# Optimization experiments

Hardware: AMD Instinct MI355X
Metric: run time of the kernel (lower is better)

The kernel has to match this reference:

```python
import jax, jax.numpy as jnp
import numpy as np

EPS = 1e-5

def setup_inputs() -> dict:
    key = jax.random.key(0)
    ks = jax.random.split(key, 12)
    B, S = 48, 1024
    x = jax.random.normal(ks[0], (3, B, S, 3), dtype=jnp.float32)
    # stacked per-band projection weights: index 0=a, 1=b, 2=c
    WQ = jax.random.normal(ks[1], (3, 3, 3), dtype=jnp.float32) * 0.3
    bQ = jax.random.normal(ks[2], (3, 3), dtype=jnp.float32) * 0.1
    WK = jax.random.normal(ks[3], (3, 3, 3), dtype=jnp.float32) * 0.3
    bK = jax.random.normal(ks[4], (3, 3), dtype=jnp.float32) * 0.1
    WV = jax.random.normal(ks[5], (3, 3, 3), dtype=jnp.float32) * 0.3
    bV = jax.random.normal(ks[6], (3, 3), dtype=jnp.float32) * 0.1
    bn_gamma = jnp.ones((9,), dtype=jnp.float32)
    bn_beta = jnp.zeros((9,), dtype=jnp.float32)
    fc_w = jax.random.normal(ks[7], (3, 9), dtype=jnp.float32) * 0.3
    fc_b = jax.random.normal(ks[8], (3,), dtype=jnp.float32) * 0.1
    return dict(x=x, WQ=WQ, bQ=bQ, WK=WK, bK=bK, WV=WV, bV=bV,
                bn_gamma=bn_gamma, bn_beta=bn_beta, fc_w=fc_w, fc_b=fc_b)

def _attn(Q, K, V):
    # Q,K,V: (B, S, 3)
    scores = jnp.einsum('bsd,btd->bst', Q, K) / jnp.sqrt(jnp.float32(3.0))
    w = jax.nn.softmax(scores, axis=-1)
    return jnp.einsum('bst,btd->bsd', w, V)

def reference(x, WQ, bQ, WK, bK, WV, bV, bn_gamma, bn_beta, fc_w, fc_b):
    # x: (3, B, S, 3) -> per-band xs[n]: (B, S, 3)
    xs = x  # band axis already leading
    # per-band projections: Q[n] = xs[n] @ WQ[n].T + bQ[n]
    Q = jnp.einsum('nbsd,ned->nbse', xs, WQ) + bQ[:, None, None, :]
    K = jnp.einsum('nbsd,ned->nbse', xs, WK) + bK[:, None, None, :]
    V = jnp.einsum('nbsd,ned->nbse', xs, WV) + bV[:, None, None, :]
    a1 = _attn(Q[2], K[0], V[1])  # Q_c, K_a, V_b
    a2 = _attn(Q[0], K[1], V[2])  # Q_a, K_b, V_c
    a3 = _attn(Q[1], K[2], V[0])  # Q_b, K_c, V_a
    out = jnp.concatenate([a1, a2, a3], axis=-1)  # (B, S, 9)
    flat = out.reshape(-1, 9)
    # BatchNorm1d (training-mode batch statistics, biased variance)
    mean = jnp.mean(flat, axis=0)
    var = jnp.var(flat, axis=0)
    normed = (flat - mean) / jnp.sqrt(var + EPS) * bn_gamma + bn_beta
    y = normed @ fc_w.T + fc_b  # (B*S, 3)
    return y.reshape(-1, 3, 3)
```

## Files before the change

### kernel.cpp

```cpp
#include <hip/hip_runtime.h>
#include <math.h>

#define BB 48
#define SS 1024
#define NCB (3 * BB)
#define NROW (BB * SS)
#define NBLK2 (NROW / 256)

typedef float f32x2 __attribute__((ext_vector_type(2)));


template <int KSv>
__global__ __launch_bounds__(256) void mbfca_attn(
    const float* __restrict__ x,
    const float* __restrict__ WQ, const float* __restrict__ bQ,
    const float* __restrict__ WK, const float* __restrict__ bK,
    const float* __restrict__ WV, const float* __restrict__ bV,
    float* __restrict__ part)
{
    constexpr int SSK = SS / KSv;
    const int bid   = blockIdx.x;
    const int slice = bid % KSv;
    const int cb    = bid / KSv;
    const int c     = cb / BB;
    const int b     = cb % BB;
    const int kband = c;
    const int vband = (c + 1) % 3;
    const int qband = (c + 2) % 3;

    __shared__ __align__(16) float Ksm[3][SSK];
    __shared__ __align__(16) float Vsm[3][SSK];

    const int tid = threadIdx.x;

    float wk[9], wv[9], wq[9], bk[3], bv[3], bq[3];
    #pragma unroll
    for (int i = 0; i < 9; ++i) {
        wk[i] = WK[kband * 9 + i];
        wv[i] = WV[vband * 9 + i];
        wq[i] = WQ[qband * 9 + i];
    }
    #pragma unroll
    for (int i = 0; i < 3; ++i) {
        bk[i] = bK[kband * 3 + i];
        bv[i] = bV[vband * 3 + i];
        bq[i] = bQ[qband * 3 + i];
    }

    const float* xk = x + (size_t)(kband * BB + b) * SS * 3;
    const float* xv = x + (size_t)(vband * BB + b) * SS * 3;
    const float* xq = x + (size_t)(qband * BB + b) * SS * 3;

    for (int t = tid; t < SSK; t += 256) {
        const int tk = slice * SSK + t;
        float a0 = xk[tk * 3 + 0], a1 = xk[tk * 3 + 1], a2 = xk[tk * 3 + 2];
        Ksm[0][t] = wk[0] * a0 + wk[1] * a1 + wk[2] * a2 + bk[0];
        Ksm[1][t] = wk[3] * a0 + wk[4] * a1 + wk[5] * a2 + bk[1];
        Ksm[2][t] = wk[6] * a0 + wk[7] * a1 + wk[8] * a2 + bk[2];
        float c0 = xv[tk * 3 + 0], c1 = xv[tk * 3 + 1], c2 = xv[tk * 3 + 2];
        Vsm[0][t] = wv[0] * c0 + wv[1] * c1 + wv[2] * c2 + bv[0];
        Vsm[1][t] = wv[3] * c0 + wv[4] * c1 + wv[5] * c2 + bv[1];
        Vsm[2][t] = wv[6] * c0 + wv[7] * c1 + wv[8] * c2 + bv[2];
    }
    __syncthreads();

    const float qscale = 0.57735026918962576f * 1.4426950408889634f;
    f32x2 qp0[4], qp1[4], qp2[4];
    {
        const float4* xq4 = reinterpret_cast<const float4*>(xq + 12 * tid);
        float4 A = xq4[0], B4 = xq4[1], C4 = xq4[2];
        float a[12] = {A.x, A.y, A.z, A.w, B4.x, B4.y, B4.z, B4.w,
                       C4.x, C4.y, C4.z, C4.w};
        #pragma unroll
        for (int j = 0; j < 4; ++j) {
            float a0 = a[j * 3 + 0], a1 = a[j * 3 + 1], a2 = a[j * 3 + 2];
            float t0 = (wq[0] * a0 + wq[1] * a1 + wq[2] * a2 + bq[0]) * qscale;
            float t1 = (wq[3] * a0 + wq[4] * a1 + wq[5] * a2 + bq[1]) * qscale;
            float t2 = (wq[6] * a0 + wq[7] * a1 + wq[8] * a2 + bq[2]) * qscale;
            qp0[j] = (f32x2){t0, t0};
            qp1[j] = (f32x2){t1, t1};
            qp2[j] = (f32x2){t2, t2};
        }
    }

    f32x2 lac[4], a0[4], a1[4], a2[4];
    #pragma unroll
    for (int j = 0; j < 4; ++j) {
        lac[j] = (f32x2){0.f, 0.f};
        a0[j]  = (f32x2){0.f, 0.f};
        a1[j]  = (f32x2){0.f, 0.f};
        a2[j]  = (f32x2){0.f, 0.f};
    }

    const float4* K0 = reinterpret_cast<const float4*>(&Ksm[0][0]);
    const float4* K1 = reinterpret_cast<const float4*>(&Ksm[1][0]);
    const float4* K2 = reinterpret_cast<const float4*>(&Ksm[2][0]);
    const float4* V0 = reinterpret_cast<const float4*>(&Vsm[0][0]);
    const float4* V1 = reinterpret_cast<const float4*>(&Vsm[1][0]);
    const float4* V2 = reinterpret_cast<const float4*>(&Vsm[2][0]);

    for (int t4 = 0; t4 < SSK / 4; ++t4) {
        float4 k0 = K0[t4], k1 = K1[t4], k2 = K2[t4];
        float4 v0 = V0[t4], v1 = V1[t4], v2 = V2[t4];
        f32x2 k0l = {k0.x, k0.y}, k0h = {k0.z, k0.w};
        f32x2 k1l = {k1.x, k1.y}, k1h = {k1.z, k1.w};
        f32x2 k2l = {k2.x, k2.y}, k2h = {k2.z, k2.w};
        f32x2 v0l = {v0.x, v0.y}, v0h = {v0.z, v0.w};
        f32x2 v1l = {v1.x, v1.y}, v1h = {v1.z, v1.w};
        f32x2 v2l = {v2.x, v2.y}, v2h = {v2.z, v2.w};
        #pragma unroll
        for (int j = 0; j < 4; ++j) {
            f32x2 sl = qp0[j] * k0l + qp1[j] * k1l + qp2[j] * k2l;
            f32x2 sh = qp0[j] * k0h + qp1[j] * k1h + qp2[j] * k2h;
            f32x2 pl, ph;
            pl.x = __builtin_amdgcn_exp2f(sl.x);
            pl.y = __builtin_amdgcn_exp2f(sl.y);
            ph.x = __builtin_amdgcn_exp2f(sh.x);
            ph.y = __builtin_amdgcn_exp2f(sh.y);
            lac[j] += pl + ph;
            a0[j]  += pl * v0l + ph * v0h;
            a1[j]  += pl * v1l + ph * v1h;
            a2[j]  += pl * v2l + ph * v2h;
        }
    }

    float4* dst = reinterpret_cast<float4*>(part) +
                  ((size_t)(slice * NCB + cb) * SS + 4 * tid);
    #pragma unroll
    for (int j = 0; j < 4; ++j)
        dst[j] = make_float4(a0[j].x + a0[j].y,
                             a1[j].x + a1[j].y,
                             a2[j].x + a2[j].y,
                             lac[j].x + lac[j].y);
}

template <int KSv>
__global__ __launch_bounds__(256) void mbfca_stats(
    float* __restrict__ part, float* __restrict__ partial)
{
    const int r = blockIdx.x * 256 + threadIdx.x;
    const int b = r >> 10, s = r & 1023;
    __shared__ float red[4][18];

    float sums[18];
    #pragma unroll
    for (int k = 0; k < 18; ++k) sums[k] = 0.f;

    float4* p4 = reinterpret_cast<float4*>(part);
    #pragma unroll
    for (int c = 0; c < 3; ++c) {
        const int cb = c * BB + b;
        float4 t = make_float4(0.f, 0.f, 0.f, 0.f);
        #pragma unroll
        for (int sl = 0; sl < KSv; ++sl) {
            float4 u = p4[(size_t)(sl * NCB + cb) * SS + s];
            t.x += u.x; t.y += u.y; t.z += u.z; t.w += u.w;
        }
        float inv = 1.0f / t.w;
        float o0 = t.x * inv, o1 = t.y * inv, o2 = t.z * inv;
        p4[(size_t)cb * SS + s] = make_float4(o0, o1, o2, 0.f);
        sums[3 * c + 0] = o0;          sums[3 * c + 1] = o1;          sums[3 * c + 2] = o2;
        sums[9 + 3 * c + 0] = o0 * o0; sums[9 + 3 * c + 1] = o1 * o1; sums[9 + 3 * c + 2] = o2 * o2;
    }

    #pragma unroll
    for (int off = 32; off >= 1; off >>= 1)
        #pragma unroll
        for (int k = 0; k < 18; ++k)
            sums[k] += __shfl_xor(sums[k], off, 64);

    const int tid = threadIdx.x;
    if ((tid & 63) == 0) {
        #pragma unroll
        for (int k = 0; k < 18; ++k) red[tid >> 6][k] = sums[k];
    }
    __syncthreads();
    if (tid < 18)
        partial[blockIdx.x * 18 + tid] =
            red[0][tid] + red[1][tid] + red[2][tid] + red[3][tid];
}

__global__ __launch_bounds__(256) void mbfca_bnfc(
    const float* __restrict__ part, const float* __restrict__ partial,
    const float* __restrict__ gamma, const float* __restrict__ beta,
    const float* __restrict__ fcw, const float* __restrict__ fcb,
    float* __restrict__ out)
{
    __shared__ float red[4][18];
    __shared__ float accs[18];
    const int tid = threadIdx.x;

    float sums[18];
    #pragma unroll
    for (int k = 0; k < 18; ++k) sums[k] = 0.f;
    if (tid < NBLK2) {
        #pragma unroll
        for (int k = 0; k < 18; ++k) sums[k] = partial[tid * 18 + k];
    }
    #pragma unroll
    for (int off = 32; off >= 1; off >>= 1)
        #pragma unroll
        for (int k = 0; k < 18; ++k)
            sums[k] += __shfl_xor(sums[k], off, 64);
    if ((tid & 63) == 0) {
        #pragma unroll
        for (int k = 0; k < 18; ++k) red[tid >> 6][k] = sums[k];
    }
    __syncthreads();
    if (tid < 18)
        accs[tid] = red[0][tid] + red[1][tid] + red[2][tid] + red[3][tid];
    __syncthreads();

    const int r = blockIdx.x * 256 + tid;
    const int b = r >> 10, s = r & 1023;
    const float invN = 1.0f / (float)NROW;

    float sc[9], sh[9];
    #pragma unroll
    for (int ch = 0; ch < 9; ++ch) {
        float mean = accs[ch] * invN;
        float var  = accs[9 + ch] * invN - mean * mean;
        float sfac = gamma[ch] * rsqrtf(var + 1e-5f);
        sc[ch] = sfac;
        sh[ch] = beta[ch] - mean * sfac;
    }

    const float4* p4 = reinterpret_cast<const float4*>(part);
    float y0 = fcb[0], y1 = fcb[1], y2 = fcb[2];
    #pragma unroll
    for (int c = 0; c < 3; ++c) {
        const int cb = c * BB + b;
        float4 t = p4[(size_t)cb * SS + s];
        float o[3] = {t.x, t.y, t.z};
        #pragma unroll
        for (int e = 0; e < 3; ++e) {
            float n = o[e] * sc[3 * c + e] + sh[3 * c + e];
            y0 += n * fcw[3 * c + e];
            y1 += n * fcw[9 + 3 * c + e];
            y2 += n * fcw[18 + 3 * c + e];
        }
    }
    out[r * 3 + 0] = y0;
    out[r * 3 + 1] = y1;
    out[r * 3 + 2] = y2;
}

template <int KSv>
static void run_pipeline(const float* x, const float* WQ, const float* bQ,
                         const float* WK, const float* bK,
                         const float* WV, const float* bV,
                         const float* gamma, const float* beta,
                         const float* fcw, const float* fcb,
                         float* part, float* out, hipStream_t stream)
{
    float* partial = part + (size_t)KSv * NCB * SS * 4;
    mbfca_attn<KSv><<<dim3(NCB * KSv), dim3(256), 0, stream>>>(
        x, WQ, bQ, WK, bK, WV, bV, part);
    mbfca_stats<KSv><<<dim3(NBLK2), dim3(256), 0, stream>>>(part, partial);
    mbfca_bnfc<<<dim3(NBLK2), dim3(256), 0, stream>>>(
        part, partial, gamma, beta, fcw, fcb, out);
}

extern "C" void kernel_launch(void* const* d_in, const int* in_sizes, int n_in,
                              void* d_out, int out_size, void* d_ws, size_t ws_size,
                              hipStream_t stream)
{
    const float* x     = (const float*)d_in[0];
    const float* WQ    = (const float*)d_in[1];
    const float* bQv   = (const float*)d_in[2];
    const float* WK    = (const float*)d_in[3];
    const float* bKv   = (const float*)d_in[4];
    const float* WV    = (const float*)d_in[5];
    const float* bVv   = (const float*)d_in[6];
    const float* gamma = (const float*)d_in[7];
    const float* beta  = (const float*)d_in[8];
    const float* fcw   = (const float*)d_in[9];
    const float* fcb   = (const float*)d_in[10];

    float* part = (float*)d_ws;

    const size_t tail = (size_t)NBLK2 * 18 * sizeof(float);
    const size_t need16 = (size_t)16 * NCB * SS * 4 * sizeof(float) + tail;
    const size_t need8  = (size_t)8  * NCB * SS * 4 * sizeof(float) + tail;

    if (ws_size >= need16) {
        run_pipeline<16>(x, WQ, bQv, WK, bKv, WV, bVv, gamma, beta, fcw, fcb,
                         part, (float*)d_out, stream);
    } else if (ws_size >= need8) {
        run_pipeline<8>(x, WQ, bQv, WK, bKv, WV, bVv, gamma, beta, fcw, fcb,
                        part, (float*)d_out, stream);
    } else {
        run_pipeline<4>(x, WQ, bQv, WK, bKv, WV, bVv, gamma, beta, fcw, fcb,
                        part, (float*)d_out, stream);
    }
}
```

Before: 53.52 us.

## Split Q/K/V projection into separate kernel and read K/V from global

Adds a projection kernel that computes Q (pre-scaled), K and V once per band and batch into a workspace. The attention kernel then reads them directly from global memory instead of recomputing the projections into shared memory in every key slice, and drops the shared-memory staging and its barrier. This targets the redundant per-slice projection work and the synchronisation. It costs an extra kernel launch, extra global traffic, and key reads that now go through cache instead of LDS. The key split also changes from 16 to 8 slices, and the inner loop gets an unroll of 2.

```diff
diff --git a/kernel.cpp b/kernel.cpp
--- a/kernel.cpp
+++ b/kernel.cpp
@@ -9,79 +9,81 @@
 
 typedef float f32x2 __attribute__((ext_vector_type(2)));
 
-
-template <int KSv>
-__global__ __launch_bounds__(256) void mbfca_attn(
+#define PROJ_ONE ((size_t)NCB * 3 * SS)
+
+__global__ __launch_bounds__(256) void mbfca_proj(
     const float* __restrict__ x,
     const float* __restrict__ WQ, const float* __restrict__ bQ,
     const float* __restrict__ WK, const float* __restrict__ bK,
     const float* __restrict__ WV, const float* __restrict__ bV,
-    float* __restrict__ part)
+    float* __restrict__ Qh, float* __restrict__ Kh, float* __restrict__ Vh)
+{
+    const int bid   = blockIdx.x;
+    const int which = bid % 3;
+    const int cb    = bid / 3;
+    const int c     = cb / BB;
+    const int b     = cb % BB;
+    const int band  = (which == 0) ? (c + 2) % 3 : (which == 1) ? c : (c + 1) % 3;
+    const float* W  = (which == 0) ? WQ : (which == 1) ? WK : WV;
+    const float* Bi = (which == 0) ? bQ : (which == 1) ? bK : bV;
+    const float scale = (which == 0)
+        ? 0.57735026918962576f * 1.4426950408889634f : 1.0f;
+    float* dst = ((which == 0) ? Qh : (which == 1) ? Kh : Vh)
+                 + (size_t)cb * 3 * SS;
+    const float* src = x + (size_t)(band * BB + b) * SS * 3;
+
+    float w[9], bb[3];
+    #pragma unroll
+    for (int i = 0; i < 9; ++i) w[i] = W[band * 9 + i] * scale;
+    #pragma unroll
+    for (int i = 0; i < 3; ++i) bb[i] = Bi[band * 3 + i] * scale;
+
+    const int tid = threadIdx.x;
+    const float4* s4 = reinterpret_cast<const float4*>(src + 12 * tid);
+    float4 A = s4[0], B4 = s4[1], C4 = s4[2];
+    float a[12] = {A.x, A.y, A.z, A.w, B4.x, B4.y, B4.z, B4.w,
+                   C4.x, C4.y, C4.z, C4.w};
+    float o[3][4];
+    #pragma unroll
+    for (int j = 0; j < 4; ++j) {
+        float a0 = a[3 * j], a1 = a[3 * j + 1], a2 = a[3 * j + 2];
+        o[0][j] = w[0] * a0 + w[1] * a1 + w[2] * a2 + bb[0];
+        o[1][j] = w[3] * a0 + w[4] * a1 + w[5] * a2 + bb[1];
+        o[2][j] = w[6] * a0 + w[7] * a1 + w[8] * a2 + bb[2];
+    }
+    #pragma unroll
+    for (int p = 0; p < 3; ++p)
+        reinterpret_cast<float4*>(dst + (size_t)p * SS)[tid] =
+            make_float4(o[p][0], o[p][1], o[p][2], o[p][3]);
+}
+
+template <int KSv>
+__global__ __launch_bounds__(256) void mbfca_attn(
+    const float* __restrict__ Qh, const float* __restrict__ Kh,
+    const float* __restrict__ Vh, float* __restrict__ part)
 {
     constexpr int SSK = SS / KSv;
     const int bid   = blockIdx.x;
     const int slice = bid % KSv;
     const int cb    = bid / KSv;
-    const int c     = cb / BB;
-    const int b     = cb % BB;
-    const int kband = c;
-    const int vband = (c + 1) % 3;
-    const int qband = (c + 2) % 3;
-
-    __shared__ __align__(16) float Ksm[3][SSK];
-    __shared__ __align__(16) float Vsm[3][SSK];
-
-    const int tid = threadIdx.x;
-
-    float wk[9], wv[9], wq[9], bk[3], bv[3], bq[3];
-    #pragma unroll
-    for (int i = 0; i < 9; ++i) {
-        wk[i] = WK[kband * 9 + i];
-        wv[i] = WV[vband * 9 + i];
-        wq[i] = WQ[qband * 9 + i];
-    }
-    #pragma unroll
-    for (int i = 0; i < 3; ++i) {
-        bk[i] = bK[kband * 3 + i];
-        bv[i] = bV[vband * 3 + i];
-        bq[i] = bQ[qband * 3 + i];
-    }
-
-    const float* xk = x + (size_t)(kband * BB + b) * SS * 3;
-    const float* xv = x + (size_t)(vband * BB + b) * SS * 3;
-    const float* xq = x + (size_t)(qband * BB + b) * SS * 3;
-
-    for (int t = tid; t < SSK; t += 256) {
-        const int tk = slice * SSK + t;
-        float a0 = xk[tk * 3 + 0], a1 = xk[tk * 3 + 1], a2 = xk[tk * 3 + 2];
-        Ksm[0][t] = wk[0] * a0 + wk[1] * a1 + wk[2] * a2 + bk[0];
-        Ksm[1][t] = wk[3] * a0 + wk[4] * a1 + wk[5] * a2 + bk[1];
-        Ksm[2][t] = wk[6] * a0 + wk[7] * a1 + wk[8] * a2 + bk[2];
-        float c0 = xv[tk * 3 + 0], c1 = xv[tk * 3 + 1], c2 = xv[tk * 3 + 2];
-        Vsm[0][t] = wv[0] * c0 + wv[1] * c1 + wv[2] * c2 + bv[0];
-        Vsm[1][t] = wv[3] * c0 + wv[4] * c1 + wv[5] * c2 + bv[1];
-        Vsm[2][t] = wv[6] * c0 + wv[7] * c1 + wv[8] * c2 + bv[2];
-    }
-    __syncthreads();
-
-    const float qscale = 0.57735026918962576f * 1.4426950408889634f;
-    f32x2 qp0[4], qp1[4], qp2[4];
-    {
-        const float4* xq4 = reinterpret_cast<const float4*>(xq + 12 * tid);
-        float4 A = xq4[0], B4 = xq4[1], C4 = xq4[2];
-        float a[12] = {A.x, A.y, A.z, A.w, B4.x, B4.y, B4.z, B4.w,
-                       C4.x, C4.y, C4.z, C4.w};
-        #pragma unroll
-        for (int j = 0; j < 4; ++j) {
-            float a0 = a[j * 3 + 0], a1 = a[j * 3 + 1], a2 = a[j * 3 + 2];
-            float t0 = (wq[0] * a0 + wq[1] * a1 + wq[2] * a2 + bq[0]) * qscale;
-            float t1 = (wq[3] * a0 + wq[4] * a1 + wq[5] * a2 + bq[1]) * qscale;
-            float t2 = (wq[6] * a0 + wq[7] * a1 + wq[8] * a2 + bq[2]) * qscale;
-            qp0[j] = (f32x2){t0, t0};
-            qp1[j] = (f32x2){t1, t1};
-            qp2[j] = (f32x2){t2, t2};
-        }
-    }
+    const int tid   = threadIdx.x;
+
+    const float* qbase = Qh + (size_t)cb * 3 * SS;
+    float4 qv0 = reinterpret_cast<const float4*>(qbase + 0 * SS)[tid];
+    float4 qv1 = reinterpret_cast<const float4*>(qbase + 1 * SS)[tid];
+    float4 qv2 = reinterpret_cast<const float4*>(qbase + 2 * SS)[tid];
+    f32x2 qp0[4] = {{qv0.x,qv0.x},{qv0.y,qv0.y},{qv0.z,qv0.z},{qv0.w,qv0.w}};
+    f32x2 qp1[4] = {{qv1.x,qv1.x},{qv1.y,qv1.y},{qv1.z,qv1.z},{qv1.w,qv1.w}};
+    f32x2 qp2[4] = {{qv2.x,qv2.x},{qv2.y,qv2.y},{qv2.z,qv2.z},{qv2.w,qv2.w}};
+
+    const float* kbase = Kh + (size_t)cb * 3 * SS + slice * SSK;
+    const float* vbase = Vh + (size_t)cb * 3 * SS + slice * SSK;
+    const float4* K0 = reinterpret_cast<const float4*>(kbase + 0 * SS);
+    const float4* K1 = reinterpret_cast<const float4*>(kbase + 1 * SS);
+    const float4* K2 = reinterpret_cast<const float4*>(kbase + 2 * SS);
+    const float4* V0 = reinterpret_cast<const float4*>(vbase + 0 * SS);
+    const float4* V1 = reinterpret_cast<const float4*>(vbase + 1 * SS);
+    const float4* V2 = reinterpret_cast<const float4*>(vbase + 2 * SS);
 
     f32x2 lac[4], a0[4], a1[4], a2[4];
     #pragma unroll
@@ -92,13 +94,7 @@
         a2[j]  = (f32x2){0.f, 0.f};
     }
 
-    const float4* K0 = reinterpret_cast<const float4*>(&Ksm[0][0]);
-    const float4* K1 = reinterpret_cast<const float4*>(&Ksm[1][0]);
-    const float4* K2 = reinterpret_cast<const float4*>(&Ksm[2][0]);
-    const float4* V0 = reinterpret_cast<const float4*>(&Vsm[0][0]);
-    const float4* V1 = reinterpret_cast<const float4*>(&Vsm[1][0]);
-    const float4* V2 = reinterpret_cast<const float4*>(&Vsm[2][0]);
-
+    #pragma unroll 2
     for (int t4 = 0; t4 < SSK / 4; ++t4) {
         float4 k0 = K0[t4], k1 = K1[t4], k2 = K2[t4];
         float4 v0 = V0[t4], v1 = V1[t4], v2 = V2[t4];
@@ -251,11 +247,18 @@
                          const float* WV, const float* bV,
                          const float* gamma, const float* beta,
                          const float* fcw, const float* fcb,
-                         float* part, float* out, hipStream_t stream)
-{
-    float* partial = part + (size_t)KSv * NCB * SS * 4;
+                         float* ws, float* out, hipStream_t stream)
+{
+    float* part = ws;
+    float* Qh   = part + (size_t)KSv * NCB * SS * 4;
+    float* Kh   = Qh + PROJ_ONE;
+    float* Vh   = Kh + PROJ_ONE;
+    float* partial = Vh + PROJ_ONE;
+
+    mbfca_proj<<<dim3(NCB * 3), dim3(256), 0, stream>>>(
+        x, WQ, bQ, WK, bK, WV, bV, Qh, Kh, Vh);
     mbfca_attn<KSv><<<dim3(NCB * KSv), dim3(256), 0, stream>>>(
-        x, WQ, bQ, WK, bK, WV, bV, part);
+        Qh, Kh, Vh, part);
     mbfca_stats<KSv><<<dim3(NBLK2), dim3(256), 0, stream>>>(part, partial);
     mbfca_bnfc<<<dim3(NBLK2), dim3(256), 0, stream>>>(
         part, partial, gamma, beta, fcw, fcb, out);
@@ -277,20 +280,17 @@
     const float* fcw   = (const float*)d_in[9];
     const float* fcb   = (const float*)d_in[10];
 
-    float* part = (float*)d_ws;
-
-    const size_t tail = (size_t)NBLK2 * 18 * sizeof(float);
-    const size_t need16 = (size_t)16 * NCB * SS * 4 * sizeof(float) + tail;
-    const size_t need8  = (size_t)8  * NCB * SS * 4 * sizeof(float) + tail;
-
-    if (ws_size >= need16) {
-        run_pipeline<16>(x, WQ, bQv, WK, bKv, WV, bVv, gamma, beta, fcw, fcb,
-                         part, (float*)d_out, stream);
-    } else if (ws_size >= need8) {
+    float* ws = (float*)d_ws;
+
+    const size_t tail = 3 * PROJ_ONE * sizeof(float)
+                      + (size_t)NBLK2 * 18 * sizeof(float);
+    const size_t need8 = (size_t)8 * NCB * SS * 4 * sizeof(float) + tail;
+
+    if (ws_size >= need8) {
         run_pipeline<8>(x, WQ, bQv, WK, bKv, WV, bVv, gamma, beta, fcw, fcb,
-                        part, (float*)d_out, stream);
+                        ws, (float*)d_out, stream);
     } else {
         run_pipeline<4>(x, WQ, bQv, WK, bKv, WV, bVv, gamma, beta, fcw, fcb,
-                        part, (float*)d_out, stream);
-    }
-}
+                        ws, (float*)d_out, stream);
+    }
+}
```

Measured after the change: 58.82 us (median of 2 runs). 9.9% more time.
